# Kernel optimization log

Measured on AMD Instinct MI355X. Metric: run time of the kernel, lower is better.

The kernel has to match this reference:

```python
import jax, jax.numpy as jnp
import numpy as np

NDIM = 1024
NHEAD = 16
B, T = 4, 2048
EPS = 1e-05
GELU_C = np.sqrt(2.0 / np.pi).astype(np.float32)


def new_gelu(x):
    return 0.5 * x * (1.0 + jnp.tanh(GELU_C * (x + 0.044715 * x ** 3)))


def layer_norm(x, w, b):
    mu = jnp.mean(x, axis=-1, keepdims=True)
    var = jnp.var(x, axis=-1, keepdims=True)
    return (x - mu) * jax.lax.rsqrt(var + EPS) * w + b


def setup_inputs() -> dict:
    key = jax.random.key(0)
    ks = jax.random.split(key, 8)
    d, dff = NDIM, 4 * NDIM
    s = 0.02
    return {
        "x": jax.random.normal(ks[0], (B, T, d), jnp.float32),
        "ln1_w": jnp.ones((d,), jnp.float32),
        "ln1_b": jnp.zeros((d,), jnp.float32),
        "w_attn": jax.random.normal(ks[1], (d, 3 * d), jnp.float32) * s,
        "b_attn": jnp.zeros((3 * d,), jnp.float32),
        "w_proj": jax.random.normal(ks[2], (d, d), jnp.float32) * s,
        "b_proj": jnp.zeros((d,), jnp.float32),
        "ln2_w": jnp.ones((d,), jnp.float32),
        "ln2_b": jnp.zeros((d,), jnp.float32),
        "w_fc": jax.random.normal(ks[3], (d, dff), jnp.float32) * s,
        "b_fc": jnp.zeros((dff,), jnp.float32),
        "w_fc2": jax.random.normal(ks[4], (dff, d), jnp.float32) * s,
        "b_fc2": jnp.zeros((d,), jnp.float32),
    }


def reference(x, ln1_w, ln1_b, w_attn, b_attn, w_proj, b_proj,
              ln2_w, ln2_b, w_fc, b_fc, w_fc2, b_fc2):
    Bx, Tx, C = x.shape
    hd = C // NHEAD
    # --- attention ---
    h = layer_norm(x, ln1_w, ln1_b)
    qkv = h @ w_attn + b_attn                       # [B,T,3C]
    q, k, v = jnp.split(qkv, 3, axis=-1)
    q = q.reshape(Bx, Tx, NHEAD, hd).transpose(0, 2, 1, 3)  # [B,H,T,hd]
    k = k.reshape(Bx, Tx, NHEAD, hd).transpose(0, 2, 1, 3)
    v = v.reshape(Bx, Tx, NHEAD, hd).transpose(0, 2, 1, 3)
    att = jnp.einsum('bhqd,bhkd->bhqk', q, k) * (1.0 / np.sqrt(hd).astype(np.float32))
    causal = jnp.tril(jnp.ones((Tx, Tx), bool))
    att = jnp.where(causal[None, None], att, jnp.float32(-jnp.inf))
    att = jax.nn.softmax(att, axis=-1)
    y = jnp.einsum('bhqk,bhkd->bhqd', att, v)
    y = y.transpose(0, 2, 1, 3).reshape(Bx, Tx, C)
    x = x + y @ w_proj + b_proj
    # --- MLP ---
    h2 = layer_norm(x, ln2_w, ln2_b)
    x = x + new_gelu(h2 @ w_fc + b_fc) @ w_fc2 + b_fc2
    return x
```

## Files before the change

kernel.cpp:

```cpp
#include <hip/hip_runtime.h>

typedef __attribute__((ext_vector_type(8))) short short8;
typedef __attribute__((ext_vector_type(8))) unsigned short ushort8;
typedef __attribute__((ext_vector_type(4))) float f32x4;
typedef __attribute__((ext_vector_type(16))) float f32x16;
typedef __attribute__((ext_vector_type(2))) unsigned int uint2v;
typedef unsigned int uint32;

__device__ __forceinline__ unsigned short f2bf(float f){
  union { float f; unsigned int u; } x; x.f = f;
  unsigned int u = x.u;
  u += 0x7fffu + ((u >> 16) & 1u);
  return (unsigned short)(u >> 16);
}
__device__ __forceinline__ float bf2f(unsigned short s){
  union { float f; unsigned int u; } x; x.u = ((uint32)s) << 16; return x.f;
}

typedef __attribute__((address_space(1))) void gvoid;
typedef __attribute__((address_space(3))) void lvoid;
__device__ __forceinline__ void gload_lds16(const void* g, void* l){
  __builtin_amdgcn_global_load_lds((gvoid*)g, (lvoid*)l, 16, 0, 0);
}

__device__ __forceinline__ f32x4 mfma_bf16(short8 a, short8 b, f32x4 c){
  return __builtin_amdgcn_mfma_f32_16x16x32_bf16(a, b, c, 0, 0, 0);
}
__device__ __forceinline__ f32x16 mfma32(short8 a, short8 b, f32x16 c){
  return __builtin_amdgcn_mfma_f32_32x32x16_bf16(a, b, c, 0, 0, 0);
}

__device__ __forceinline__ uint32 cvtpk_bf(float lo, float hi){
  uint32 r;
  asm("v_cvt_pk_bf16_f32 %0, %1, %2" : "=v"(r) : "v"(lo), "v"(hi));
  return r;
}
__device__ __forceinline__ void plswap(uint32& a, uint32& b){
  auto r = __builtin_amdgcn_permlane32_swap(a, b, false, false);
  a = r[0]; b = r[1];
}

#if __has_builtin(__builtin_amdgcn_exp2f)
__device__ __forceinline__ float exp2g(float x){ return __builtin_amdgcn_exp2f(x); }
#else
__device__ __forceinline__ float exp2g(float x){ return exp2f(x); }
#endif

__device__ __forceinline__ f32x16 zero16(){
  f32x16 z;
  #pragma unroll
  for (int i = 0; i < 16; i++) z[i] = 0.0f;
  return z;
}

__global__ __launch_bounds__(256) void wtrans_kernel(
    const float* __restrict__ w, unsigned short* __restrict__ wt, int K, int N)
{
  __shared__ float tile[32][33];
  const int n0 = blockIdx.x * 32;
  const int k0 = blockIdx.y * 32;
  const int t = threadIdx.x;
  #pragma unroll
  for (int i = 0; i < 4; i++){
    const int e = t + i * 256;
    const int r = e >> 5, c = e & 31;
    tile[r][c] = w[(size_t)(k0 + r) * N + n0 + c];
  }
  __syncthreads();
  #pragma unroll
  for (int i = 0; i < 4; i++){
    const int e = t + i * 256;
    const int r = e >> 5, c = e & 31;
    wt[(size_t)(n0 + r) * K + k0 + c] = f2bf(tile[c][r]);
  }
}

__global__ __launch_bounds__(256) void vtrans_kernel(
    const unsigned short* __restrict__ qkv, unsigned short* __restrict__ vt)
{
  __shared__ unsigned short tile[32][33];
  const int bh = blockIdx.z;
  const int b = bh >> 4, h = bh & 15;
  const int t0 = blockIdx.x * 32;
  const int f0 = blockIdx.y * 32;
  const int t = threadIdx.x;
  #pragma unroll
  for (int i = 0; i < 4; i++){
    const int e = t + i * 256;
    const int r = e >> 5, c = e & 31;
    tile[r][c] = qkv[(size_t)(b * 2048 + t0 + r) * 3072 + 2048 + h * 64 + f0 + c];
  }
  __syncthreads();
  #pragma unroll
  for (int i = 0; i < 4; i++){
    const int e = t + i * 256;
    const int r = e >> 5, c = e & 31;
    vt[((size_t)bh * 64 + f0 + r) * 2048 + t0 + c] = tile[c][r];
  }
}

__global__ __launch_bounds__(256) void ln_kernel(
    const float* __restrict__ x, const float* __restrict__ w, const float* __restrict__ b,
    unsigned short* __restrict__ out)
{
  const int row = blockIdx.x;
  const int t = threadIdx.x;
  const float4 v = ((const float4*)(x + (size_t)row * 1024))[t];
  float s  = v.x + v.y + v.z + v.w;
  float s2 = v.x * v.x + v.y * v.y + v.z * v.z + v.w * v.w;
  #pragma unroll
  for (int off = 32; off > 0; off >>= 1){
    s  += __shfl_xor(s, off);
    s2 += __shfl_xor(s2, off);
  }
  __shared__ float ps[8];
  const int wid = t >> 6;
  if ((t & 63) == 0){ ps[wid] = s; ps[4 + wid] = s2; }
  __syncthreads();
  s  = ps[0] + ps[1] + ps[2] + ps[3];
  s2 = ps[4] + ps[5] + ps[6] + ps[7];
  const float mu  = s * (1.0f / 1024.0f);
  const float var = s2 * (1.0f / 1024.0f) - mu * mu;
  const float rs  = rsqrtf(var + 1e-5f);
  const float4 wv = ((const float4*)w)[t];
  const float4 bv = ((const float4*)b)[t];
  ushort4 ov;
  ov.x = f2bf((v.x - mu) * rs * wv.x + bv.x);
  ov.y = f2bf((v.y - mu) * rs * wv.y + bv.y);
  ov.z = f2bf((v.z - mu) * rs * wv.z + bv.z);
  ov.w = f2bf((v.w - mu) * rs * wv.w + bv.w);
  ((ushort4*)(out + (size_t)row * 1024))[t] = ov;
}

#define EPI_BF16   0
#define EPI_RESF32 1
#define EPI_GELU   2

template<int EPI, int BN>
__global__ __launch_bounds__(512, 2) void gemm4_kernel(
    const unsigned short* __restrict__ A,
    const unsigned short* __restrict__ BT,
    const float* __restrict__ bias,
    const float* __restrict__ res,
    void* __restrict__ outp,
    int M, int N, int K)
{
  constexpr int MI   = (BN == 256) ? 8 : 4;
  constexpr int SP   = MI / 4;
  constexpr int NBL  = BN / 128;
  constexpr int WN   = (BN == 256) ? 4 : 2;
  constexpr int WROWS= (BN == 256) ? 128 : 64;
  constexpr int ASL  = 16384;
  constexpr int SLOT = ASL + BN * 64;
  __shared__ __align__(16) char lds[4 * SLOT];

  const int nwg = gridDim.x;
  const int bid = blockIdx.x;
  const int wg = (bid & 7) * (nwg >> 3) + (bid >> 3);
  const int NTile = N / BN;
  const int mt = wg / NTile;
  const int nti = wg - mt * NTile;
  const int m0 = mt << 8;
  const int n0 = nti * BN;

  const int tid = threadIdx.x;
  const int lane = tid & 63;
  const int wid = tid >> 6;
  const int wv_m = wid / WN;
  const int wv_n = wid % WN;
  const int fr = lane & 15;
  const int fg = lane >> 4;

  const unsigned short* aSrc[2];
  int aDst[2];
  #pragma unroll
  for (int l = 0; l < 2; l++){
    const int s = l * 512 + tid;
    const int r = s >> 2, c = s & 3;
    aSrc[l] = A + (size_t)(m0 + r) * K + ((c ^ ((r >> 1) & 3)) << 3);
    aDst[l] = s * 16;
  }
  const unsigned short* bSrc[NBL];
  int bDst[NBL];
  #pragma unroll
  for (int l = 0; l < NBL; l++){
    const int s = l * 512 + tid;
    const int r = s >> 2, c = s & 3;
    bSrc[l] = BT + (size_t)(n0 + r) * K + ((c ^ ((r >> 1) & 3)) << 3);
    bDst[l] = ASL + s * 16;
  }

  int aOff[MI], bOff[4];
  #pragma unroll
  for (int mi = 0; mi < MI; mi++){
    const int row = wv_m * WROWS + mi * 16 + fr;
    aOff[mi] = row * 64 + ((fg ^ ((row >> 1) & 3)) << 4);
  }
  #pragma unroll
  for (int nj = 0; nj < 4; nj++){
    const int row = wv_n * 64 + nj * 16 + fr;
    bOff[nj] = ASL + row * 64 + ((fg ^ ((row >> 1) & 3)) << 4);
  }

  f32x4 acc[MI][4];
  #pragma unroll
  for (int i = 0; i < MI; i++)
    #pragma unroll
    for (int j = 0; j < 4; j++) acc[i][j] = (f32x4){0.f, 0.f, 0.f, 0.f};

#define STAGE_A(sl, slot) do { \
    gload_lds16(aSrc[0] + (size_t)(sl) * 32, lds + (slot) + aDst[0]); \
    gload_lds16(aSrc[1] + (size_t)(sl) * 32, lds + (slot) + aDst[1]); \
  } while (0)
#define STAGE_B(sl, slot) do { \
    gload_lds16(bSrc[0] + (size_t)(sl) * 32, lds + (slot) + bDst[0]); \
    if (NBL == 2) gload_lds16(bSrc[1] + (size_t)(sl) * 32, lds + (slot) + bDst[1]); \
  } while (0)

  const int NS = K >> 5;

  STAGE_A(0, 0);        STAGE_B(0, 0);
  STAGE_A(1, SLOT);     STAGE_B(1, SLOT);
  STAGE_A(2, 2 * SLOT); STAGE_B(2, 2 * SLOT);
  if (BN == 256) asm volatile("s_waitcnt vmcnt(8)" ::: "memory");
  else           asm volatile("s_waitcnt vmcnt(6)" ::: "memory");
  __builtin_amdgcn_s_barrier();

  for (int s = 0; s < NS; s++){
    const int ss = (s & 3) * SLOT;
    const int sg = ((s + 3) & 3) * SLOT;
    const bool pf = (s + 3 < NS);
    short8 bF[4];
    #pragma unroll
    for (int sp = 0; sp < SP; sp++){
      short8 aF[4];
      #pragma unroll
      for (int i = 0; i < 4; i++)
        aF[i] = *(const short8*)(lds + ss + aOff[sp * 4 + i]);
      if (sp == 0){
        #pragma unroll
        for (int nj = 0; nj < 4; nj++)
          bF[nj] = *(const short8*)(lds + ss + bOff[nj]);
      }
      if (pf){
        if (SP == 2){
          if (sp == 0) STAGE_A(s + 3, sg);
          else         STAGE_B(s + 3, sg);
        } else {
          STAGE_A(s + 3, sg);
          STAGE_B(s + 3, sg);
        }
      }
      __builtin_amdgcn_s_barrier();
      asm volatile("s_waitcnt lgkmcnt(0)" ::: "memory");
      __builtin_amdgcn_sched_barrier(0);
      __builtin_amdgcn_s_setprio(1);
      #pragma unroll
      for (int i = 0; i < 4; i++)
        #pragma unroll
        for (int nj = 0; nj < 4; nj++)
          acc[sp * 4 + i][nj] = mfma_bf16(aF[i], bF[nj], acc[sp * 4 + i][nj]);
      __builtin_amdgcn_s_setprio(0);
      if (sp == SP - 1){
        if (s + 3 < NS){
          if (BN == 256) asm volatile("s_waitcnt vmcnt(8)" ::: "memory");
          else           asm volatile("s_waitcnt vmcnt(6)" ::: "memory");
        } else if (s + 2 < NS){
          if (BN == 256) asm volatile("s_waitcnt vmcnt(4)" ::: "memory");
          else           asm volatile("s_waitcnt vmcnt(3)" ::: "memory");
        } else if (s + 1 < NS){
          asm volatile("s_waitcnt vmcnt(0)" ::: "memory");
        }
      }
      __builtin_amdgcn_s_barrier();
    }
  }
#undef STAGE_A
#undef STAGE_B

  #pragma unroll
  for (int mi = 0; mi < MI; mi++){
    const int mrow = m0 + wv_m * WROWS + mi * 16 + fg * 4;
    #pragma unroll
    for (int nj = 0; nj < 4; nj++){
      const int ncol = n0 + wv_n * 64 + nj * 16 + fr;
      const float bv = bias[ncol];
      #pragma unroll
      for (int r2 = 0; r2 < 4; r2++){
        const size_t idx = (size_t)(mrow + r2) * N + ncol;
        float v = acc[mi][nj][r2] + bv;
        if (EPI == EPI_RESF32){
          ((float*)outp)[idx] = v + res[idx];
        } else if (EPI == EPI_GELU){
          const float tt = tanhf(0.7978845608028654f * (v + 0.044715f * v * v * v));
          ((unsigned short*)outp)[idx] = f2bf(0.5f * v * (1.0f + tt));
        } else {
          ((unsigned short*)outp)[idx] = f2bf(v);
        }
      }
    }
  }
}

template<bool MASK>
__device__ __forceinline__ void attn_tile(
    const unsigned short* __restrict__ Kc, const unsigned short* __restrict__ Vc,
    const short8 (&qf)[4], int kvbase, int qg, int l31, int hi,
    float& m_r, float& lsum, f32x16& Oa, f32x16& Ob)
{
  f32x16 Sa = zero16();
  f32x16 Sb = zero16();
  const int xb = l31 & 7;
  #pragma unroll
  for (int kk = 0; kk < 4; kk++){
    const int x = kk * 2 + hi;
    const short8 k0 = *(const short8*)((const char*)Kc + l31 * 128 + ((x ^ xb) << 4));
    const short8 k1 = *(const short8*)((const char*)Kc + (l31 + 32) * 128 + ((x ^ xb) << 4));
    Sa = mfma32(k0, qf[kk], Sa);
    Sb = mfma32(k1, qf[kk], Sb);
  }
  if (MASK){
    #pragma unroll
    for (int r = 0; r < 16; r++){
      const int kva = kvbase + (r & 3) + 8 * (r >> 2) + 4 * hi;
      Sa[r] = (kva > qg)      ? -1e30f : Sa[r];
      Sb[r] = (kva + 32 > qg) ? -1e30f : Sb[r];
    }
  }
  float tmax = Sa[0];
  #pragma unroll
  for (int r = 1; r < 16; r++) tmax = fmaxf(tmax, Sa[r]);
  #pragma unroll
  for (int r = 0; r < 16; r++) tmax = fmaxf(tmax, Sb[r]);
  tmax = fmaxf(tmax, __shfl_xor(tmax, 32));
  if (__any(tmax > m_r + 10.0f)){
    const float mn = fmaxf(m_r, tmax);
    const float sc = exp2g(m_r - mn);
    m_r = mn;
    lsum *= sc;
    #pragma unroll
    for (int r = 0; r < 16; r++){ Oa[r] *= sc; Ob[r] *= sc; }
  }
  float rs = 0.0f;
  #pragma unroll
  for (int r = 0; r < 16; r++){
    Sa[r] = exp2g(Sa[r] - m_r); rs += Sa[r];
    Sb[r] = exp2g(Sb[r] - m_r); rs += Sb[r];
  }
  rs += __shfl_xor(rs, 32);
  lsum += rs;

  short8 pf[4];
  {
    uint32 a0 = cvtpk_bf(Sa[0], Sa[1]),   b0 = cvtpk_bf(Sa[4], Sa[5]);
    uint32 a1 = cvtpk_bf(Sa[2], Sa[3]),   b1 = cvtpk_bf(Sa[6], Sa[7]);
    plswap(a0, b0); plswap(a1, b1);
    uint32 a2 = cvtpk_bf(Sa[8], Sa[9]),   b2 = cvtpk_bf(Sa[12], Sa[13]);
    uint32 a3 = cvtpk_bf(Sa[10], Sa[11]), b3 = cvtpk_bf(Sa[14], Sa[15]);
    plswap(a2, b2); plswap(a3, b3);
    union { uint32 u[4]; short8 s; } m0, m1;
    m0.u[0] = a0; m0.u[1] = a1; m0.u[2] = b0; m0.u[3] = b1;
    m1.u[0] = a2; m1.u[1] = a3; m1.u[2] = b2; m1.u[3] = b3;
    pf[0] = m0.s; pf[1] = m1.s;
  }
  {
    uint32 a0 = cvtpk_bf(Sb[0], Sb[1]),   b0 = cvtpk_bf(Sb[4], Sb[5]);
    uint32 a1 = cvtpk_bf(Sb[2], Sb[3]),   b1 = cvtpk_bf(Sb[6], Sb[7]);
    plswap(a0, b0); plswap(a1, b1);
    uint32 a2 = cvtpk_bf(Sb[8], Sb[9]),   b2 = cvtpk_bf(Sb[12], Sb[13]);
    uint32 a3 = cvtpk_bf(Sb[10], Sb[11]), b3 = cvtpk_bf(Sb[14], Sb[15]);
    plswap(a2, b2); plswap(a3, b3);
    union { uint32 u[4]; short8 s; } m0, m1;
    m0.u[0] = a0; m0.u[1] = a1; m0.u[2] = b0; m0.u[3] = b1;
    m1.u[0] = a2; m1.u[1] = a3; m1.u[2] = b2; m1.u[3] = b3;
    pf[2] = m0.s; pf[3] = m1.s;
  }
  #pragma unroll
  for (int kk = 0; kk < 4; kk++){
    const int x = kk * 2 + hi;
    const short8 v0 = *(const short8*)((const char*)Vc + l31 * 128 + ((x ^ xb) << 4));
    const short8 v1 = *(const short8*)((const char*)Vc + (l31 + 32) * 128 + ((x ^ xb) << 4));
    Oa = mfma32(v0, pf[kk], Oa);
    Ob = mfma32(v1, pf[kk], Ob);
  }
}

__global__ __launch_bounds__(256) void attn_kernel(
    const unsigned short* __restrict__ qkv,
    const unsigned short* __restrict__ vt,
    unsigned short* __restrict__ y)
{
  __shared__ __align__(16) unsigned short Klds[2][4096];
  __shared__ __align__(16) unsigned short Vlds[2][4096];
  const int bid = blockIdx.x;
  const int bh = bid & 63;
  const int qb_i = bid >> 6;
  const int b = bh >> 4, h = bh & 15;
  const int qb0 = qb_i * 128;
  const int tid = threadIdx.x;
  const int w = tid >> 6;
  const int lane = tid & 63;
  const int l31 = lane & 31;
  const int hi = lane >> 5;

  const int qrow_g = b * 2048 + qb0 + w * 32 + l31;
  const unsigned short* qp = qkv + (size_t)qrow_g * 3072 + h * 64;
  short8 qf[4];
  #pragma unroll
  for (int kk = 0; kk < 4; kk++){
    short8 raw = *(const short8*)&qp[kk * 16 + hi * 8];
    #pragma unroll
    for (int j = 0; j < 8; j++)
      qf[kk][j] = (short)f2bf(bf2f((unsigned short)raw[j]) * 0.18033688011112042f);
  }

  const int sr = tid >> 3;
  const int ce = ((tid & 7) ^ (sr & 7)) * 8;
  const unsigned short* kb = qkv + (size_t)(b * 2048) * 3072 + 1024 + h * 64;
  const unsigned short* vb = vt + (size_t)bh * 64 * 2048;

  f32x16 Oa = zero16(), Ob = zero16();
  float m_r = -1e30f, lsum = 0.0f;
  const int qmin = qb0 + w * 32;
  const int qmax = qmin + 31;
  const int qg = qmin + l31;
  const int nkv = (qb0 >> 6) + 2;

#define STAGE(t, bb) do { \
    const size_t kro = (size_t)((t) * 64 + sr) * 3072; \
    gload_lds16(kb + kro + ce,                         (char*)&Klds[bb][0] + tid * 16); \
    gload_lds16(kb + kro + (size_t)32 * 3072 + ce,     (char*)&Klds[bb][0] + 4096 + tid * 16); \
    gload_lds16(vb + (size_t)sr * 2048 + (t) * 64 + ce,        (char*)&Vlds[bb][0] + tid * 16); \
    gload_lds16(vb + (size_t)(sr + 32) * 2048 + (t) * 64 + ce, (char*)&Vlds[bb][0] + 4096 + tid * 16); \
  } while (0)

  STAGE(0, 0);
  __syncthreads();
  int cur = 0;
  for (int kvt = 0; kvt < nkv; kvt++){
    if (kvt + 1 < nkv){
      if (cur) STAGE(kvt + 1, 0); else STAGE(kvt + 1, 1);
    }
    if (kvt * 64 <= qmax){
      if (kvt * 64 + 63 <= qmin)
        attn_tile<false>(Klds[cur], Vlds[cur], qf, kvt * 64, qg, l31, hi, m_r, lsum, Oa, Ob);
      else
        attn_tile<true >(Klds[cur], Vlds[cur], qf, kvt * 64, qg, l31, hi, m_r, lsum, Oa, Ob);
    }
    __syncthreads();
    cur ^= 1;
  }
#undef STAGE

  const float inv = 1.0f / lsum;
  unsigned short* yp = y + (size_t)qrow_g * 1024 + h * 64;
  #pragma unroll
  for (int c2 = 0; c2 < 4; c2++){
    uint2v da, db;
    da.x = cvtpk_bf(Oa[4 * c2 + 0] * inv, Oa[4 * c2 + 1] * inv);
    da.y = cvtpk_bf(Oa[4 * c2 + 2] * inv, Oa[4 * c2 + 3] * inv);
    *(uint2v*)&yp[8 * c2 + 4 * hi] = da;
    db.x = cvtpk_bf(Ob[4 * c2 + 0] * inv, Ob[4 * c2 + 1] * inv);
    db.y = cvtpk_bf(Ob[4 * c2 + 2] * inv, Ob[4 * c2 + 3] * inv);
    *(uint2v*)&yp[32 + 8 * c2 + 4 * hi] = db;
  }
}

extern "C" void kernel_launch(void* const* d_in, const int* in_sizes, int n_in,
                              void* d_out, int out_size, void* d_ws, size_t ws_size,
                              hipStream_t stream)
{
  const float* x      = (const float*)d_in[0];
  const float* ln1_w  = (const float*)d_in[1];
  const float* ln1_b  = (const float*)d_in[2];
  const float* w_attn = (const float*)d_in[3];
  const float* b_attn = (const float*)d_in[4];
  const float* w_proj = (const float*)d_in[5];
  const float* b_proj = (const float*)d_in[6];
  const float* ln2_w  = (const float*)d_in[7];
  const float* ln2_b  = (const float*)d_in[8];
  const float* w_fc   = (const float*)d_in[9];
  const float* b_fc   = (const float*)d_in[10];
  const float* w_fc2  = (const float*)d_in[11];
  const float* b_fc2  = (const float*)d_in[12];

  char* ws = (char*)d_ws;
  unsigned short* wbT_attn = (unsigned short*)(ws + 0);
  unsigned short* wbT_proj = (unsigned short*)(ws + 6291456);
  unsigned short* wbT_fc   = (unsigned short*)(ws + 8388608);
  unsigned short* wbT_fc2  = (unsigned short*)(ws + 16777216);
  unsigned short* h_bf     = (unsigned short*)(ws + 25165824);
  unsigned short* qkv_bf   = (unsigned short*)(ws + 41943040);
  unsigned short* vt_bf    = (unsigned short*)(ws + 92274688);
  unsigned short* g_bf     = (unsigned short*)(ws + 41943040);
  unsigned short* y_bf     = (unsigned short*)(ws + 109051904);
  float*          x1       = (float*)(ws + 125829120);
  float* outf = (float*)d_out;

  wtrans_kernel<<<dim3(3072/32, 1024/32), 256, 0, stream>>>(w_attn, wbT_attn, 1024, 3072);
  wtrans_kernel<<<dim3(1024/32, 1024/32), 256, 0, stream>>>(w_proj, wbT_proj, 1024, 1024);
  wtrans_kernel<<<dim3(4096/32, 1024/32), 256, 0, stream>>>(w_fc,   wbT_fc,   1024, 4096);
  wtrans_kernel<<<dim3(1024/32, 4096/32), 256, 0, stream>>>(w_fc2,  wbT_fc2,  4096, 1024);

  ln_kernel<<<8192, 256, 0, stream>>>(x, ln1_w, ln1_b, h_bf);
  gemm4_kernel<EPI_BF16, 256><<<384, 512, 0, stream>>>(
      h_bf, wbT_attn, b_attn, nullptr, qkv_bf, 8192, 3072, 1024);
  vtrans_kernel<<<dim3(64, 2, 64), 256, 0, stream>>>(qkv_bf, vt_bf);
  attn_kernel<<<1024, 256, 0, stream>>>(qkv_bf, vt_bf, y_bf);
  gemm4_kernel<EPI_RESF32, 128><<<256, 512, 0, stream>>>(
      y_bf, wbT_proj, b_proj, x, x1, 8192, 1024, 1024);
  ln_kernel<<<8192, 256, 0, stream>>>(x1, ln2_w, ln2_b, h_bf);
  gemm4_kernel<EPI_GELU, 256><<<512, 512, 0, stream>>>(
      h_bf, wbT_fc, b_fc, nullptr, g_bf, 8192, 4096, 1024);
  gemm4_kernel<EPI_RESF32, 128><<<256, 512, 0, stream>>>(
      g_bf, wbT_fc2, b_fc2, x1, outf, 8192, 1024, 4096);
}
```

Measured before the change: 392.5 us.

## Add 128x256 three-stage GEMM kernel for QKV and FC, fast exp-based GELU

Adds a new gemm5 kernel: 256-thread workgroups computing 128x256 tiles with a BK=32 three-slot LDS ring fed by direct global-to-LDS loads, a swizzled layout, and an XCD-aware block remap. It is used for the QKV and FC GEMMs in place of the 512-thread gemm4 and is meant to raise occupancy and improve pipelining. Separately, the GELU epilogue replaces tanhf with an exp2/rcp formulation to cut transcendental cost. The smaller K step means more barriers per tile, and the fast GELU form could lose precision or overflow for large inputs.

```diff
diff --git a/kernel.cpp b/kernel.cpp
--- a/kernel.cpp
+++ b/kernel.cpp
@@ -45,6 +45,17 @@
 #else
 __device__ __forceinline__ float exp2g(float x){ return exp2f(x); }
 #endif
+#if __has_builtin(__builtin_amdgcn_rcpf)
+__device__ __forceinline__ float rcpg(float x){ return __builtin_amdgcn_rcpf(x); }
+#else
+__device__ __forceinline__ float rcpg(float x){ return 1.0f / x; }
+#endif
+
+__device__ __forceinline__ float gelu_fast(float v){
+  const float u = 0.7978845608028654f * (v + 0.044715f * v * v * v);
+  const float E = exp2g(2.8853900817779268f * u);
+  return v - v * rcpg(1.0f + E);
+}
 
 __device__ __forceinline__ f32x16 zero16(){
   f32x16 z;
@@ -135,6 +146,137 @@
 #define EPI_BF16   0
 #define EPI_RESF32 1
 #define EPI_GELU   2
+
+template<int EPI>
+__global__ __launch_bounds__(256, 2) void gemm5_kernel(
+    const unsigned short* __restrict__ A,
+    const unsigned short* __restrict__ BT,
+    const float* __restrict__ bias,
+    const float* __restrict__ res,
+    void* __restrict__ outp,
+    int M, int N, int K)
+{
+  constexpr int SLOT = 24576;
+  __shared__ __align__(16) char lds[3 * SLOT];
+
+  const int nwg = gridDim.x;
+  const int bid = blockIdx.x;
+  const int wg = (bid & 7) * (nwg >> 3) + (bid >> 3);
+  const int NT = N >> 8;
+  const int mt = wg / NT;
+  const int nti = wg - mt * NT;
+  const int m0 = mt << 7;
+  const int n0 = nti << 8;
+
+  const int tid = threadIdx.x;
+  const int lane = tid & 63;
+  const int wid = tid >> 6;
+  const int fr = lane & 15;
+  const int fg = lane >> 4;
+
+  const unsigned short* aSrc[2]; int aDst[2];
+  #pragma unroll
+  for (int l = 0; l < 2; l++){
+    const int s = l * 256 + tid;
+    const int r = s >> 2, c = s & 3;
+    aSrc[l] = A + (size_t)(m0 + r) * K + ((c ^ ((r >> 1) & 3)) << 3);
+    aDst[l] = s * 16;
+  }
+  const unsigned short* bSrc[4]; int bDst[4];
+  #pragma unroll
+  for (int l = 0; l < 4; l++){
+    const int s = l * 256 + tid;
+    const int r = s >> 2, c = s & 3;
+    bSrc[l] = BT + (size_t)(n0 + r) * K + ((c ^ ((r >> 1) & 3)) << 3);
+    bDst[l] = 8192 + s * 16;
+  }
+
+  int aOff[8], bOff[4];
+  #pragma unroll
+  for (int mi = 0; mi < 8; mi++){
+    const int row = mi * 16 + fr;
+    aOff[mi] = row * 64 + ((fg ^ ((row >> 1) & 3)) << 4);
+  }
+  #pragma unroll
+  for (int nj = 0; nj < 4; nj++){
+    const int row = wid * 64 + nj * 16 + fr;
+    bOff[nj] = 8192 + row * 64 + ((fg ^ ((row >> 1) & 3)) << 4);
+  }
+
+  f32x4 acc[8][4];
+  #pragma unroll
+  for (int i = 0; i < 8; i++)
+    #pragma unroll
+    for (int j = 0; j < 4; j++) acc[i][j] = (f32x4){0.f, 0.f, 0.f, 0.f};
+
+#define STAGE5(sl, slot) do { \
+    gload_lds16(aSrc[0] + (size_t)(sl) * 32, lds + (slot) + aDst[0]); \
+    gload_lds16(aSrc[1] + (size_t)(sl) * 32, lds + (slot) + aDst[1]); \
+    gload_lds16(bSrc[0] + (size_t)(sl) * 32, lds + (slot) + bDst[0]); \
+    gload_lds16(bSrc[1] + (size_t)(sl) * 32, lds + (slot) + bDst[1]); \
+    gload_lds16(bSrc[2] + (size_t)(sl) * 32, lds + (slot) + bDst[2]); \
+    gload_lds16(bSrc[3] + (size_t)(sl) * 32, lds + (slot) + bDst[3]); \
+  } while (0)
+
+  const int NS = K >> 5;
+
+  STAGE5(0, 0);
+  STAGE5(1, SLOT);
+  asm volatile("s_waitcnt vmcnt(6)" ::: "memory");
+  __builtin_amdgcn_s_barrier();
+  asm volatile("" ::: "memory");
+
+  int cs = 0, cg = 2 * SLOT;
+  for (int s = 0; s < NS; s++){
+    short8 aF[8], bF[4];
+    #pragma unroll
+    for (int mi = 0; mi < 8; mi++)
+      aF[mi] = *(const short8*)(lds + cs + aOff[mi]);
+    #pragma unroll
+    for (int nj = 0; nj < 4; nj++)
+      bF[nj] = *(const short8*)(lds + cs + bOff[nj]);
+    if (s + 2 < NS) STAGE5(s + 2, cg);
+    #pragma unroll
+    for (int mi = 0; mi < 8; mi++)
+      #pragma unroll
+      for (int nj = 0; nj < 4; nj++)
+        acc[mi][nj] = mfma_bf16(aF[mi], bF[nj], acc[mi][nj]);
+
+    if (s + 2 < NS){
+      asm volatile("s_waitcnt vmcnt(6)" ::: "memory");
+    } else if (s + 1 < NS){
+      asm volatile("s_waitcnt vmcnt(0)" ::: "memory");
+    }
+    __builtin_amdgcn_s_barrier();
+    asm volatile("" ::: "memory");
+
+    cs += SLOT; if (cs == 3 * SLOT) cs = 0;
+    cg += SLOT; if (cg == 3 * SLOT) cg = 0;
+  }
+#undef STAGE5
+
+  #pragma unroll
+  for (int mi = 0; mi < 8; mi++){
+    const int mrow = m0 + mi * 16 + fg * 4;
+    #pragma unroll
+    for (int nj = 0; nj < 4; nj++){
+      const int ncol = n0 + wid * 64 + nj * 16 + fr;
+      const float bv = bias[ncol];
+      #pragma unroll
+      for (int r2 = 0; r2 < 4; r2++){
+        const size_t idx = (size_t)(mrow + r2) * N + ncol;
+        float v = acc[mi][nj][r2] + bv;
+        if (EPI == EPI_RESF32){
+          ((float*)outp)[idx] = v + res[idx];
+        } else if (EPI == EPI_GELU){
+          ((unsigned short*)outp)[idx] = f2bf(gelu_fast(v));
+        } else {
+          ((unsigned short*)outp)[idx] = f2bf(v);
+        }
+      }
+    }
+  }
+}
 
 template<int EPI, int BN>
 __global__ __launch_bounds__(512, 2) void gemm4_kernel(
@@ -292,8 +434,7 @@
         if (EPI == EPI_RESF32){
           ((float*)outp)[idx] = v + res[idx];
         } else if (EPI == EPI_GELU){
-          const float tt = tanhf(0.7978845608028654f * (v + 0.044715f * v * v * v));
-          ((unsigned short*)outp)[idx] = f2bf(0.5f * v * (1.0f + tt));
+          ((unsigned short*)outp)[idx] = f2bf(gelu_fast(v));
         } else {
           ((unsigned short*)outp)[idx] = f2bf(v);
         }
@@ -503,14 +644,14 @@
   wtrans_kernel<<<dim3(1024/32, 4096/32), 256, 0, stream>>>(w_fc2,  wbT_fc2,  4096, 1024);
 
   ln_kernel<<<8192, 256, 0, stream>>>(x, ln1_w, ln1_b, h_bf);
-  gemm4_kernel<EPI_BF16, 256><<<384, 512, 0, stream>>>(
+  gemm5_kernel<EPI_BF16><<<768, 256, 0, stream>>>(
       h_bf, wbT_attn, b_attn, nullptr, qkv_bf, 8192, 3072, 1024);
   vtrans_kernel<<<dim3(64, 2, 64), 256, 0, stream>>>(qkv_bf, vt_bf);
   attn_kernel<<<1024, 256, 0, stream>>>(qkv_bf, vt_bf, y_bf);
   gemm4_kernel<EPI_RESF32, 128><<<256, 512, 0, stream>>>(
       y_bf, wbT_proj, b_proj, x, x1, 8192, 1024, 1024);
   ln_kernel<<<8192, 256, 0, stream>>>(x1, ln2_w, ln2_b, h_bf);
-  gemm4_kernel<EPI_GELU, 256><<<512, 512, 0, stream>>>(
+  gemm5_kernel<EPI_GELU><<<1024, 256, 0, stream>>>(
       h_bf, wbT_fc, b_fc, nullptr, g_bf, 8192, 4096, 1024);
   gemm4_kernel<EPI_RESF32, 128><<<256, 512, 0, stream>>>(
       g_bf, wbT_fc2, b_fc2, x1, outf, 8192, 1024, 4096);
```

Result: faster. 359.3 us (-8.5%).
